# Performance work log

Hardware: AMD Instinct MI355X
Metric: run time of the kernel (lower is better)

## Reference

```python
import jax, jax.numpy as jnp
import numpy as np

N_NODES = 50000
N_EDGES = 650000
NEG_SLOPE = 0.2


def gat_conv(x, src, dst, W, a_src, a_dst, bias, concat):
    """PyG-style GATConv (eval mode, self-loops already included in src/dst).
    x: [N, F_in], W: [F_in, H*C], a_src/a_dst: [H, C], bias: [H*C] or [C]."""
    N = x.shape[0]
    H, C = a_src.shape
    h = (x @ W).reshape(N, H, C)                      # [N, H, C]
    al_src = (h * a_src).sum(-1)                      # [N, H]
    al_dst = (h * a_dst).sum(-1)                      # [N, H]
    logits = jax.nn.leaky_relu(al_src[src] + al_dst[dst], NEG_SLOPE)  # [E, H]
    # segment softmax over destination neighborhoods
    m = jax.ops.segment_max(logits, dst, num_segments=N)
    m = jnp.where(jnp.isfinite(m), m, 0.0)
    e = jnp.exp(logits - m[dst])
    s = jax.ops.segment_sum(e, dst, num_segments=N)
    alpha = e / (s[dst] + 1e-16)                      # [E, H]
    msg = alpha[:, :, None] * h[src]                  # [E, H, C]
    out = jax.ops.segment_sum(msg, dst, num_segments=N)  # [N, H, C]
    out = out.reshape(N, H * C) if concat else out.mean(axis=1)
    return out + bias


def setup_inputs() -> dict:
    key = jax.random.key(0)
    ks = jax.random.split(key, 16)
    IN, HID, H, OUT = 128, 64, 4, 1
    x = jax.random.normal(ks[0], (N_NODES, IN), dtype=jnp.float32)
    edge_index = jax.random.randint(ks[1], (2, N_EDGES), 0, N_NODES, dtype=jnp.int64)
    s = 0.1
    params = {
        'W1': jax.random.normal(ks[2], (IN, H * HID), dtype=jnp.float32) * s,
        'a_src1': jax.random.normal(ks[3], (H, HID), dtype=jnp.float32) * s,
        'a_dst1': jax.random.normal(ks[4], (H, HID), dtype=jnp.float32) * s,
        'b1': jnp.zeros((H * HID,), dtype=jnp.float32),
        'W2': jax.random.normal(ks[5], (H * HID, H * HID), dtype=jnp.float32) * s,
        'a_src2': jax.random.normal(ks[6], (H, HID), dtype=jnp.float32) * s,
        'a_dst2': jax.random.normal(ks[7], (H, HID), dtype=jnp.float32) * s,
        'b2': jnp.zeros((H * HID,), dtype=jnp.float32),
        'W3': jax.random.normal(ks[8], (H * HID, OUT), dtype=jnp.float32) * s,
        'a_src3': jax.random.normal(ks[9], (1, OUT), dtype=jnp.float32) * s,
        'a_dst3': jax.random.normal(ks[10], (1, OUT), dtype=jnp.float32) * s,
        'b3': jnp.zeros((OUT,), dtype=jnp.float32),
    }
    return {'x': x, 'edge_index': edge_index, **params}


def reference(x, edge_index, W1, a_src1, a_dst1, b1, W2, a_src2, a_dst2, b2, W3, a_src3, a_dst3, b3):
    N = x.shape[0]
    loops = jnp.arange(N, dtype=edge_index.dtype)
    src = jnp.concatenate([edge_index[0], loops])
    dst = jnp.concatenate([edge_index[1], loops])
    h = gat_conv(x, src, dst, W1, a_src1, a_dst1, b1, concat=True)
    h = jax.nn.elu(h)  # dropout: identity in eval mode
    h = gat_conv(h, src, dst, W2, a_src2, a_dst2, b2, concat=True)
    h = jax.nn.elu(h)
    out = gat_conv(h, src, dst, W3, a_src3, a_dst3, b3, concat=False)
    return out
```

## Files before the change

### kernel.cpp

```cpp
#include <hip/hip_runtime.h>
#include <math.h>

#define NN 50000
#define NE 650000
#define NET 700000
#define FD 256
#define NEG 0.2f
#define NB 49

static __device__ __forceinline__ float lrelu(float v){ return v > 0.f ? v : NEG*v; }

static __device__ __forceinline__ unsigned short f2bf(float f){
  union { float f; unsigned u; } v; v.f = f;
  unsigned r = v.u + 0x7fff + ((v.u >> 16) & 1);
  return (unsigned short)(r >> 16);
}
static __device__ __forceinline__ float bf2f(unsigned short h){
  union { unsigned u; float f; } v; v.u = ((unsigned)h) << 16;
  return v.f;
}
static __device__ __forceinline__ float bflo(unsigned u){ return __uint_as_float(u << 16); }
static __device__ __forceinline__ float bfhi(unsigned u){ return __uint_as_float(u & 0xffff0000u); }

static __device__ __forceinline__ void gload_lds16(const unsigned short* g, unsigned short* l){
  __builtin_amdgcn_global_load_lds(
      (const __attribute__((address_space(1))) unsigned int*)(g),
      (__attribute__((address_space(3))) unsigned int*)(l), 16, 0, 0);
}

typedef __attribute__((ext_vector_type(8))) short short8_t;
typedef __attribute__((ext_vector_type(4))) float f32x4;

#define NX (NN*128)
#define CAST_ELEMS (NX + 128*256 + 256*256)
#define CAST_BLOCKS ((CAST_ELEMS/4 + 255)/256)
#define CNT_BLOCKS ((NET + 255)/256)
__global__ void init_fused(const float* __restrict__ x, const float* __restrict__ W1,
                           const float* __restrict__ W2,
                           unsigned short* __restrict__ xh, unsigned short* __restrict__ xl,
                           unsigned short* __restrict__ bt1h, unsigned short* __restrict__ bt1l,
                           unsigned short* __restrict__ bt2h, unsigned short* __restrict__ bt2l,
                           const int* __restrict__ ei, int* __restrict__ deg){
  int b = blockIdx.x;
  if (b >= CAST_BLOCKS){
    int e = (b - CAST_BLOCKS)*256 + threadIdx.x;
    if (e < NET){
      int d = (e < NE) ? ei[NE + e] : (e - NE);
      atomicAdd(&deg[d], 1);
    }
    return;
  }
  int i = (b*256 + threadIdx.x)*4;
  if (i < NX){
    float4 f = *(const float4*)(x + i);
    ushort4 h, l;
    h.x = f2bf(f.x); l.x = f2bf(f.x - bf2f(h.x));
    h.y = f2bf(f.y); l.y = f2bf(f.y - bf2f(h.y));
    h.z = f2bf(f.z); l.z = f2bf(f.z - bf2f(h.z));
    h.w = f2bf(f.w); l.w = f2bf(f.w - bf2f(h.w));
    *(ushort4*)(xh + i) = h;
    *(ushort4*)(xl + i) = l;
    return;
  }
  int e, K;
  const float* B;
  unsigned short *bh, *bl;
  if (i < NX + 128*256){ e = i - NX; K = 128; B = W1; bh = bt1h; bl = bt1l; }
  else if (i < CAST_ELEMS){ e = i - NX - 128*256; K = 256; B = W2; bh = bt2h; bl = bt2l; }
  else return;
  int k = e >> 8, n = e & 255;
  float4 f = *(const float4*)(B + e);
  #pragma unroll
  for (int j=0;j<4;j++){
    float fv = (j==0)?f.x:(j==1)?f.y:(j==2)?f.z:f.w;
    unsigned short h = f2bf(fv);
    bh[(n+j)*K + k] = h;
    bl[(n+j)*K + k] = f2bf(fv - bf2f(h));
  }
}

__global__ void scan_block(const int* __restrict__ deg, int* __restrict__ excl, int* __restrict__ bsums){
  __shared__ int sh[256];
  int t = threadIdx.x;
  int i0 = blockIdx.x*1024 + t*4;
  int v0 = (i0+0 < NN) ? deg[i0+0] : 0;
  int v1 = (i0+1 < NN) ? deg[i0+1] : 0;
  int v2 = (i0+2 < NN) ? deg[i0+2] : 0;
  int v3 = (i0+3 < NN) ? deg[i0+3] : 0;
  int tot = v0+v1+v2+v3;
  sh[t] = tot;
  __syncthreads();
  for (int off=1; off<256; off<<=1){
    int x = (t>=off) ? sh[t-off] : 0;
    __syncthreads();
    sh[t] += x;
    __syncthreads();
  }
  int base = sh[t] - tot;
  if (i0+0 < NN) excl[i0+0] = base;
  if (i0+1 < NN) excl[i0+1] = base + v0;
  if (i0+2 < NN) excl[i0+2] = base + v0+v1;
  if (i0+3 < NN) excl[i0+3] = base + v0+v1+v2;
  if (t == 255) bsums[blockIdx.x] = sh[255];
}

__global__ void scan_add(int* __restrict__ indptr, const int* __restrict__ bsums, int* __restrict__ cursor){
  __shared__ int boff[64];
  if (threadIdx.x < 64){
    int lane = threadIdx.x;
    int v = (lane < NB) ? bsums[lane] : 0;
    int orig = v;
    for (int off=1; off<64; off<<=1){
      int u = __shfl_up(v, off);
      if (lane >= off) v += u;
    }
    boff[lane] = v - orig;
  }
  __syncthreads();
  int i = blockIdx.x*blockDim.x + threadIdx.x;
  if (i < NN){
    int v = indptr[i] + boff[i>>10];
    indptr[i] = v;
    cursor[i] = v;
  }
  if (i == 0) indptr[NN] = NET;
}

__global__ void scatter_csr(const int* __restrict__ ei, int* __restrict__ cursor, int* __restrict__ csr){
  int e = blockIdx.x*blockDim.x + threadIdx.x;
  if (e >= NET) return;
  int s, d;
  if (e < NE){ s = ei[e]; d = ei[NE+e]; } else { s = e-NE; d = e-NE; }
  int pos = atomicAdd(&cursor[d], 1);
  csr[pos] = s;
}

template<int K>
__global__ __launch_bounds__(256, 3) void gemm_mfma(const unsigned short* __restrict__ Ahg,
                                                    const unsigned short* __restrict__ Alg,
                                                    const unsigned short* __restrict__ Bth,
                                                    const unsigned short* __restrict__ Btl,
                                                    unsigned short* __restrict__ Cb,
                                                    const float* __restrict__ a_src,
                                                    const float* __restrict__ a_dst,
                                                    float* __restrict__ al,
                                                    int M){
  constexpr int ITERS = K/32;
  __shared__ unsigned short Ah[128*32], Al[128*32], Bh[128*32], Bl[128*32];
  int t = threadIdx.x;
  int wave = t >> 6, lane = t & 63;
  int wm = wave >> 1, wn = wave & 1;
  int quad = lane >> 4, l16 = lane & 15;
  int bm0 = blockIdx.y*128, bn0 = blockIdx.x*128;

  const unsigned short* gsrc = (wave==0)?Ahg:(wave==1)?Alg:(wave==2)?Bth:Btl;
  unsigned short* lbuf       = (wave==0)?Ah :(wave==1)?Al :(wave==2)?Bh :Bl;
  int sbase = (wave < 2) ? bm0 : bn0;
  int srow = lane >> 2;
  int skg  = (lane & 3) * 8;

  const unsigned short* gp[8];
  #pragma unroll
  for (int i=0;i<8;i++){
    int r = sbase + i*16 + srow;
    if (wave < 2) r = min(r, M-1);
    gp[i] = gsrc + (size_t)r*K + skg;
  }

  f32x4 acc[4][4];
  #pragma unroll
  for (int i=0;i<4;i++)
    #pragma unroll
    for (int j=0;j<4;j++) acc[i][j] = (f32x4){0.f,0.f,0.f,0.f};

  #pragma unroll
  for (int i=0;i<8;i++) gload_lds16(gp[i], lbuf + i*512);

  #pragma unroll
  for (int it=0; it<ITERS; ++it){
    __syncthreads();

    short8_t afh[4], afl[4], bfh[4], bfl[4];
    #pragma unroll
    for (int mt=0; mt<4; ++mt){
      int row = wm*64 + mt*16 + l16;
      afh[mt] = *(short8_t*)&Ah[row*32 + quad*8];
      afl[mt] = *(short8_t*)&Al[row*32 + quad*8];
    }
    #pragma unroll
    for (int nt=0; nt<4; ++nt){
      int col = wn*64 + nt*16 + l16;
      bfh[nt] = *(short8_t*)&Bh[col*32 + quad*8];
      bfl[nt] = *(short8_t*)&Bl[col*32 + quad*8];
    }
    __syncthreads();

    if (it+1 < ITERS){
      int k0 = (it+1)*32;
      #pragma unroll
      for (int i=0;i<8;i++) gload_lds16(gp[i] + k0, lbuf + i*512);
    }

    #pragma unroll
    for (int mt=0; mt<4; ++mt)
      #pragma unroll
      for (int nt=0; nt<4; ++nt){
        acc[mt][nt] = __builtin_amdgcn_mfma_f32_16x16x32_bf16(afh[mt], bfh[nt], acc[mt][nt], 0,0,0);
        acc[mt][nt] = __builtin_amdgcn_mfma_f32_16x16x32_bf16(afh[mt], bfl[nt], acc[mt][nt], 0,0,0);
        acc[mt][nt] = __builtin_amdgcn_mfma_f32_16x16x32_bf16(afl[mt], bfh[nt], acc[mt][nt], 0,0,0);
      }
  }

  int head_w = (bn0 >> 6) + wn;
  float cs[4], cd[4];
  #pragma unroll
  for (int nt=0; nt<4; ++nt){
    cs[nt] = a_src[head_w*64 + nt*16 + l16];
    cd[nt] = a_dst[head_w*64 + nt*16 + l16];
  }
  {
    float* fsc = (float*)lbuf;
    int grow = bm0 + wm*64 + lane;
    #pragma unroll
    for (int pass=0; pass<2; ++pass){
      #pragma unroll
      for (int mt=0; mt<4; ++mt)
        #pragma unroll
        for (int r=0; r<4; ++r){
          float p = 0.f;
          #pragma unroll
          for (int nt=0; nt<4; ++nt)
            p += acc[mt][nt][r] * (pass ? cd[nt] : cs[nt]);
          fsc[(mt*16 + quad*4 + r)*17 + l16] = p;
        }
      float s = 0.f;
      #pragma unroll
      for (int j=0; j<16; ++j) s += fsc[lane*17 + j];
      if (grow < M) al[grow*8 + pass*4 + head_w] = s;
    }
  }

  unsigned short* tile = lbuf;
  #pragma unroll
  for (int mt=0; mt<4; ++mt)
    #pragma unroll
    for (int r=0; r<4; ++r){
      int rl = mt*16 + quad*4 + r;
      #pragma unroll
      for (int nt=0; nt<4; ++nt)
        tile[rl*64 + nt*16 + l16] = f2bf(acc[mt][nt][r]);
    }
  int orow = lane >> 3, ocol = (lane & 7) * 8;
  #pragma unroll
  for (int it=0; it<8; ++it){
    int rl = it*8 + orow;
    int row = bm0 + wm*64 + rl;
    if (row < M){
      uint4 v = *(uint4*)&tile[rl*64 + ocol];
      *(uint4*)(Cb + (size_t)row*FD + bn0 + wn*64 + ocol) = v;
    }
  }
}

template<bool FUSE_W3>
__global__ __launch_bounds__(256) void gat_agg(const unsigned short* __restrict__ hb,
                                               const float* __restrict__ al,
                                               const int* __restrict__ indptr, const int* __restrict__ csr,
                                               const float* __restrict__ bias,
                                               unsigned short* __restrict__ outh,
                                               unsigned short* __restrict__ outl,
                                               const float* __restrict__ W3,
                                               float* __restrict__ h3){
  __shared__ float ebuf[8][128];
  __shared__ int   sbuf[8][32];
  int wave = threadIdx.x >> 6, lane = threadIdx.x & 63;
  int half = lane >> 5, l32 = lane & 31;
  int slot = wave*2 + half;
  int n = blockIdx.x*8 + slot;
  if (n >= NN) return;
  int head8 = l32 >> 3;
  int2 ip = *(const int2*)(indptr + n);
  int base = ip.x, deg = ip.y - ip.x;
  float4 ald = *(const float4*)(al + n*8 + 4);
  float* eb = &ebuf[slot][0];
  int*   sb = &sbuf[slot][0];
  const char* hp = (const char*)hb + l32*16;

  float acc[8] = {0.f,0.f,0.f,0.f,0.f,0.f,0.f,0.f};
  float4 esum = make_float4(0.f,0.f,0.f,0.f);

  for (int j0 = 0; j0 < deg; j0 += 32){
    int j = j0 + l32;
    float4 e4 = make_float4(0.f,0.f,0.f,0.f);
    int sj = 0;
    if (j < deg){
      sj = csr[base + j];
      float4 als = *(const float4*)(al + sj*8);
      e4.x = __expf(lrelu(als.x + ald.x));
      e4.y = __expf(lrelu(als.y + ald.y));
      e4.z = __expf(lrelu(als.z + ald.z));
      e4.w = __expf(lrelu(als.w + ald.w));
      esum.x += e4.x; esum.y += e4.y; esum.z += e4.z; esum.w += e4.w;
    }
    *(float4*)&eb[l32*4] = e4;
    sb[l32] = sj << 9;
    int cnt  = min(32, deg - j0);
    int cpad = (cnt + 7) & ~7;
    for (int tt = 0; tt < cpad; tt += 8){
      uint4 r[8];
      float v[8];
      #pragma unroll
      for (int q=0; q<8; ++q){
        int o = sb[tt+q];
        v[q] = eb[(tt+q)*4 + head8];
        r[q] = *(const uint4*)(hp + o);
      }
      #pragma unroll
      for (int q=0; q<8; ++q){
        acc[0]+=v[q]*bflo(r[q].x); acc[1]+=v[q]*bfhi(r[q].x);
        acc[2]+=v[q]*bflo(r[q].y); acc[3]+=v[q]*bfhi(r[q].y);
        acc[4]+=v[q]*bflo(r[q].z); acc[5]+=v[q]*bfhi(r[q].z);
        acc[6]+=v[q]*bflo(r[q].w); acc[7]+=v[q]*bfhi(r[q].w);
      }
    }
  }

  for (int off=16; off; off>>=1){
    esum.x += __shfl_xor(esum.x, off);
    esum.y += __shfl_xor(esum.y, off);
    esum.z += __shfl_xor(esum.z, off);
    esum.w += __shfl_xor(esum.w, off);
  }
  float sH = (head8==0)?esum.x:(head8==1)?esum.y:(head8==2)?esum.z:esum.w;
  float inv = 1.f/(sH + 1e-16f);
  int ch0 = l32*8;
  float4 b0 = *(const float4*)(bias + ch0);
  float4 b1 = *(const float4*)(bias + ch0 + 4);
  float o[8];
  o[0]=acc[0]*inv+b0.x; o[1]=acc[1]*inv+b0.y; o[2]=acc[2]*inv+b0.z; o[3]=acc[3]*inv+b0.w;
  o[4]=acc[4]*inv+b1.x; o[5]=acc[5]*inv+b1.y; o[6]=acc[6]*inv+b1.z; o[7]=acc[7]*inv+b1.w;
  #pragma unroll
  for (int i=0;i<8;i++) o[i] = o[i] > 0.f ? o[i] : expm1f(o[i]);

  if (FUSE_W3){
    float4 w0 = *(const float4*)(W3 + ch0);
    float4 w1 = *(const float4*)(W3 + ch0 + 4);
    float p = o[0]*w0.x + o[1]*w0.y + o[2]*w0.z + o[3]*w0.w
            + o[4]*w1.x + o[5]*w1.y + o[6]*w1.z + o[7]*w1.w;
    #pragma unroll
    for (int off=16; off; off>>=1) p += __shfl_xor(p, off);
    if (l32 == 0) h3[n] = p;
  } else {
    unsigned hi[4], lo[4];
    #pragma unroll
    for (int i=0;i<4;i++){
      unsigned short h0 = f2bf(o[2*i]),   h1 = f2bf(o[2*i+1]);
      unsigned short g0 = f2bf(o[2*i]   - bf2f(h0));
      unsigned short g1 = f2bf(o[2*i+1] - bf2f(h1));
      hi[i] = (unsigned)h0 | ((unsigned)h1 << 16);
      lo[i] = (unsigned)g0 | ((unsigned)g1 << 16);
    }
    *(uint4*)(outh + (size_t)n*FD + ch0) = make_uint4(hi[0],hi[1],hi[2],hi[3]);
    *(uint4*)(outl + (size_t)n*FD + ch0) = make_uint4(lo[0],lo[1],lo[2],lo[3]);
  }
}

__global__ __launch_bounds__(256) void gat_agg3(const float* __restrict__ h3, const int* __restrict__ indptr,
                                                const int* __restrict__ csr, const float* __restrict__ asrc,
                                                const float* __restrict__ adst, const float* __restrict__ b3,
                                                float* __restrict__ out){
  int tid = blockIdx.x*blockDim.x + threadIdx.x;
  int n = tid >> 2, sub = tid & 3;
  if (n >= NN) return;
  float as = asrc[0], ad = adst[0];
  float hd = h3[n]*ad;
  int2 ip = *(const int2*)(indptr + n);
  float s = 0.f, w = 0.f;
  for (int e = ip.x + sub; e < ip.y; e += 4){
    float hv = h3[csr[e]];
    float ee = __expf(lrelu(as*hv + hd));
    s += ee; w += ee*hv;
  }
  s += __shfl_xor(s, 1); w += __shfl_xor(w, 1);
  s += __shfl_xor(s, 2); w += __shfl_xor(w, 2);
  if (sub == 0) out[n] = w/(s + 1e-16f) + b3[0];
}

extern "C" void kernel_launch(void* const* d_in, const int* in_sizes, int n_in,
                              void* d_out, int out_size, void* d_ws, size_t ws_size,
                              hipStream_t stream){
  const float* x   = (const float*)d_in[0];
  const int*   ei  = (const int*)d_in[1];
  const float* W1  = (const float*)d_in[2];
  const float* as1 = (const float*)d_in[3];
  const float* ad1 = (const float*)d_in[4];
  const float* b1  = (const float*)d_in[5];
  const float* W2  = (const float*)d_in[6];
  const float* as2 = (const float*)d_in[7];
  const float* ad2 = (const float*)d_in[8];
  const float* b2  = (const float*)d_in[9];
  const float* W3  = (const float*)d_in[10];
  const float* as3 = (const float*)d_in[11];
  const float* ad3 = (const float*)d_in[12];
  const float* b3  = (const float*)d_in[13];
  float* outp = (float*)d_out;

  char* w = (char*)d_ws;
  size_t off = 0;
  auto alloc = [&](size_t bytes)->void*{
    void* p = w + off; off += (bytes + 255) & ~(size_t)255; return p;
  };
  unsigned short* hb  = (unsigned short*)alloc((size_t)NN*FD*2);
  unsigned short* oh  = (unsigned short*)alloc((size_t)NN*FD*2);
  unsigned short* ol  = (unsigned short*)alloc((size_t)NN*FD*2);
  unsigned short* xh  = (unsigned short*)alloc((size_t)NN*128*2);
  unsigned short* xl  = (unsigned short*)alloc((size_t)NN*128*2);
  float* al    = (float*)alloc((size_t)NN*8*4);
  int*   indptr= (int*)alloc((size_t)(NN+1)*4);
  int*   cursor= (int*)alloc((size_t)NN*4);
  int*   csr   = (int*)alloc((size_t)NET*4);
  int*   bsums = (int*)alloc(64*4);
  float* h3    = (float*)alloc((size_t)NN*4);
  unsigned short* bt1h = (unsigned short*)alloc((size_t)256*128*2);
  unsigned short* bt1l = (unsigned short*)alloc((size_t)256*128*2);
  unsigned short* bt2h = (unsigned short*)alloc((size_t)256*256*2);
  unsigned short* bt2l = (unsigned short*)alloc((size_t)256*256*2);

  hipMemsetAsync(cursor, 0, (size_t)NN*4, stream);
  init_fused<<<CAST_BLOCKS + CNT_BLOCKS, 256, 0, stream>>>(x, W1, W2, xh, xl,
                                                           bt1h, bt1l, bt2h, bt2l,
                                                           ei, cursor);
  scan_block<<<NB, 256, 0, stream>>>(cursor, indptr, bsums);
  scan_add<<<(NN+255)/256, 256, 0, stream>>>(indptr, bsums, cursor);
  scatter_csr<<<(NET+255)/256, 256, 0, stream>>>(ei, cursor, csr);

  dim3 gemm_grid(FD/128, (NN+127)/128);
  int agg_blocks = (NN+7)/8;

  gemm_mfma<128><<<gemm_grid, 256, 0, stream>>>(xh, xl, bt1h, bt1l, hb, as1, ad1, al, NN);
  gat_agg<false><<<agg_blocks, 256, 0, stream>>>(hb, al, indptr, csr, b1, oh, ol, nullptr, nullptr);
  gemm_mfma<256><<<gemm_grid, 256, 0, stream>>>(oh, ol, bt2h, bt2l, hb, as2, ad2, al, NN);
  gat_agg<true><<<agg_blocks, 256, 0, stream>>>(hb, al, indptr, csr, b2, nullptr, nullptr, W3, h3);
  gat_agg3<<<(NN*4+255)/256, 256, 0, stream>>>(h3, indptr, csr, as3, ad3, b3, outp);
}
```

Measured before the change: 343.9 us.

## Split GAT aggregation into edge-alpha pass and panel-partitioned feature gather

The GEMM now writes its bf16 output in eight 32-column panels (panel-major) instead of row-major. A new edge_alpha kernel computes the per-edge exp logits and per-node softmax sums once and stores them. A gather kernel then handles one panel per block with 16 edges in flight per wave, and layer 2 accumulates its W3 projection into h3 with atomics. The aim is a smaller per-panel working set that fits in cache and more gather parallelism. The cost is an extra kernel, the ea buffer written and read back, CSR indices reread eight times, and an extra memset.

```diff
diff --git a/kernel.cpp b/kernel.cpp
--- a/kernel.cpp
+++ b/kernel.cpp
@@ -251,117 +251,151 @@
         tile[rl*64 + nt*16 + l16] = f2bf(acc[mt][nt][r]);
     }
   int orow = lane >> 3, ocol = (lane & 7) * 8;
+  int col0 = bn0 + wn*64 + ocol;
+  int pp = col0 >> 5;
+  unsigned short* pbase = Cb + (size_t)pp*(NN*32) + (col0 & 31);
   #pragma unroll
   for (int it=0; it<8; ++it){
     int rl = it*8 + orow;
     int row = bm0 + wm*64 + rl;
     if (row < M){
       uint4 v = *(uint4*)&tile[rl*64 + ocol];
-      *(uint4*)(Cb + (size_t)row*FD + bn0 + wn*64 + ocol) = v;
-    }
-  }
-}
-
-template<bool FUSE_W3>
-__global__ __launch_bounds__(256) void gat_agg(const unsigned short* __restrict__ hb,
-                                               const float* __restrict__ al,
-                                               const int* __restrict__ indptr, const int* __restrict__ csr,
-                                               const float* __restrict__ bias,
-                                               unsigned short* __restrict__ outh,
-                                               unsigned short* __restrict__ outl,
-                                               const float* __restrict__ W3,
-                                               float* __restrict__ h3){
-  __shared__ float ebuf[8][128];
-  __shared__ int   sbuf[8][32];
+      *(uint4*)(pbase + (size_t)row*32) = v;
+    }
+  }
+}
+
+__global__ __launch_bounds__(256) void edge_alpha(const float* __restrict__ al,
+                                                  const int* __restrict__ indptr,
+                                                  const int* __restrict__ csr,
+                                                  float* __restrict__ ea,
+                                                  float* __restrict__ esum){
   int wave = threadIdx.x >> 6, lane = threadIdx.x & 63;
-  int half = lane >> 5, l32 = lane & 31;
-  int slot = wave*2 + half;
-  int n = blockIdx.x*8 + slot;
+  int n = blockIdx.x*4 + wave;
   if (n >= NN) return;
-  int head8 = l32 >> 3;
   int2 ip = *(const int2*)(indptr + n);
   int base = ip.x, deg = ip.y - ip.x;
   float4 ald = *(const float4*)(al + n*8 + 4);
-  float* eb = &ebuf[slot][0];
-  int*   sb = &sbuf[slot][0];
-  const char* hp = (const char*)hb + l32*16;
-
-  float acc[8] = {0.f,0.f,0.f,0.f,0.f,0.f,0.f,0.f};
-  float4 esum = make_float4(0.f,0.f,0.f,0.f);
-
-  for (int j0 = 0; j0 < deg; j0 += 32){
-    int j = j0 + l32;
-    float4 e4 = make_float4(0.f,0.f,0.f,0.f);
-    int sj = 0;
+  float4 es = make_float4(0.f,0.f,0.f,0.f);
+  for (int j0 = 0; j0 < deg; j0 += 64){
+    int j = j0 + lane;
     if (j < deg){
-      sj = csr[base + j];
+      int sj = csr[base + j];
       float4 als = *(const float4*)(al + sj*8);
+      float4 e4;
       e4.x = __expf(lrelu(als.x + ald.x));
       e4.y = __expf(lrelu(als.y + ald.y));
       e4.z = __expf(lrelu(als.z + ald.z));
       e4.w = __expf(lrelu(als.w + ald.w));
-      esum.x += e4.x; esum.y += e4.y; esum.z += e4.z; esum.w += e4.w;
-    }
-    *(float4*)&eb[l32*4] = e4;
-    sb[l32] = sj << 9;
-    int cnt  = min(32, deg - j0);
-    int cpad = (cnt + 7) & ~7;
-    for (int tt = 0; tt < cpad; tt += 8){
-      uint4 r[8];
-      float v[8];
-      #pragma unroll
-      for (int q=0; q<8; ++q){
-        int o = sb[tt+q];
-        v[q] = eb[(tt+q)*4 + head8];
-        r[q] = *(const uint4*)(hp + o);
+      ea[0*NET + base + j] = e4.x;
+      ea[1*NET + base + j] = e4.y;
+      ea[2*NET + base + j] = e4.z;
+      ea[3*NET + base + j] = e4.w;
+      es.x += e4.x; es.y += e4.y; es.z += e4.z; es.w += e4.w;
+    }
+  }
+  for (int off=32; off; off>>=1){
+    es.x += __shfl_xor(es.x, off);
+    es.y += __shfl_xor(es.y, off);
+    es.z += __shfl_xor(es.z, off);
+    es.w += __shfl_xor(es.w, off);
+  }
+  if (lane == 0) *(float4*)(esum + n*4) = es;
+}
+
+template<bool FUSE_W3>
+__global__ __launch_bounds__(256) void gat_gather(const unsigned short* __restrict__ hb,
+                                                  const float* __restrict__ ea,
+                                                  const float* __restrict__ esum,
+                                                  const int* __restrict__ indptr,
+                                                  const int* __restrict__ csr,
+                                                  const float* __restrict__ bias,
+                                                  unsigned short* __restrict__ outh,
+                                                  unsigned short* __restrict__ outl,
+                                                  const float* __restrict__ W3,
+                                                  float* __restrict__ h3){
+  __shared__ float ebuf[4][64];
+  __shared__ int   sbuf[4][64];
+  int wave = threadIdx.x >> 6, lane = threadIdx.x & 63;
+  int p = blockIdx.x & 7;
+  int n = (blockIdx.x >> 3)*4 + wave;
+  if (n >= NN) return;
+  int hp = p >> 1;
+  int q = lane >> 2, r16 = (lane & 3)*16;
+  int2 ip = *(const int2*)(indptr + n);
+  int base = ip.x, deg = ip.y - ip.x;
+  float inv = 1.f/(esum[n*4 + hp] + 1e-16f);
+  const char* pb = (const char*)(hb + (size_t)p*(NN*32)) + r16;
+  const float* eap = ea + (size_t)hp*NET;
+  float* eb = &ebuf[wave][0];
+  int*   sb = &sbuf[wave][0];
+
+  float acc[8] = {0.f,0.f,0.f,0.f,0.f,0.f,0.f,0.f};
+
+  for (int j0 = 0; j0 < deg; j0 += 64){
+    int j = j0 + lane;
+    float a = 0.f; int sj = 0;
+    if (j < deg){ sj = csr[base + j]; a = eap[base + j]; }
+    eb[lane] = a;
+    sb[lane] = sj << 6;
+    int cnt = min(64, deg - j0);
+    int nst = (cnt + 15) >> 4;
+    uint4 u[4]; float av[4];
+    #pragma unroll
+    for (int s=0; s<4; ++s){
+      if (s < nst){
+        int e = s*16 + q;
+        av[s] = eb[e];
+        u[s] = *(const uint4*)(pb + sb[e]);
+      } else { av[s] = 0.f; u[s] = make_uint4(0,0,0,0); }
+    }
+    #pragma unroll
+    for (int s=0; s<4; ++s){
+      acc[0]+=av[s]*bflo(u[s].x); acc[1]+=av[s]*bfhi(u[s].x);
+      acc[2]+=av[s]*bflo(u[s].y); acc[3]+=av[s]*bfhi(u[s].y);
+      acc[4]+=av[s]*bflo(u[s].z); acc[5]+=av[s]*bfhi(u[s].z);
+      acc[6]+=av[s]*bflo(u[s].w); acc[7]+=av[s]*bfhi(u[s].w);
+    }
+  }
+
+  #pragma unroll
+  for (int i=0;i<8;i++){
+    acc[i] += __shfl_xor(acc[i], 4);
+    acc[i] += __shfl_xor(acc[i], 8);
+    acc[i] += __shfl_xor(acc[i], 16);
+    acc[i] += __shfl_xor(acc[i], 32);
+  }
+
+  if (lane < 4){
+    int ch0 = p*32 + lane*8;
+    float4 b0 = *(const float4*)(bias + ch0);
+    float4 b1 = *(const float4*)(bias + ch0 + 4);
+    float o[8];
+    o[0]=acc[0]*inv+b0.x; o[1]=acc[1]*inv+b0.y; o[2]=acc[2]*inv+b0.z; o[3]=acc[3]*inv+b0.w;
+    o[4]=acc[4]*inv+b1.x; o[5]=acc[5]*inv+b1.y; o[6]=acc[6]*inv+b1.z; o[7]=acc[7]*inv+b1.w;
+    #pragma unroll
+    for (int i=0;i<8;i++) o[i] = o[i] > 0.f ? o[i] : expm1f(o[i]);
+    if (FUSE_W3){
+      float4 w0 = *(const float4*)(W3 + ch0);
+      float4 w1 = *(const float4*)(W3 + ch0 + 4);
+      float pp = o[0]*w0.x + o[1]*w0.y + o[2]*w0.z + o[3]*w0.w
+               + o[4]*w1.x + o[5]*w1.y + o[6]*w1.z + o[7]*w1.w;
+      pp += __shfl_xor(pp, 1);
+      pp += __shfl_xor(pp, 2);
+      if (lane == 0) atomicAdd(h3 + n, pp);
+    } else {
+      unsigned hi[4], lo[4];
+      #pragma unroll
+      for (int i=0;i<4;i++){
+        unsigned short h0 = f2bf(o[2*i]),   h1 = f2bf(o[2*i+1]);
+        unsigned short g0 = f2bf(o[2*i]   - bf2f(h0));
+        unsigned short g1 = f2bf(o[2*i+1] - bf2f(h1));
+        hi[i] = (unsigned)h0 | ((unsigned)h1 << 16);
+        lo[i] = (unsigned)g0 | ((unsigned)g1 << 16);
       }
-      #pragma unroll
-      for (int q=0; q<8; ++q){
-        acc[0]+=v[q]*bflo(r[q].x); acc[1]+=v[q]*bfhi(r[q].x);
-        acc[2]+=v[q]*bflo(r[q].y); acc[3]+=v[q]*bfhi(r[q].y);
-        acc[4]+=v[q]*bflo(r[q].z); acc[5]+=v[q]*bfhi(r[q].z);
-        acc[6]+=v[q]*bflo(r[q].w); acc[7]+=v[q]*bfhi(r[q].w);
-      }
-    }
-  }
-
-  for (int off=16; off; off>>=1){
-    esum.x += __shfl_xor(esum.x, off);
-    esum.y += __shfl_xor(esum.y, off);
-    esum.z += __shfl_xor(esum.z, off);
-    esum.w += __shfl_xor(esum.w, off);
-  }
-  float sH = (head8==0)?esum.x:(head8==1)?esum.y:(head8==2)?esum.z:esum.w;
-  float inv = 1.f/(sH + 1e-16f);
-  int ch0 = l32*8;
-  float4 b0 = *(const float4*)(bias + ch0);
-  float4 b1 = *(const float4*)(bias + ch0 + 4);
-  float o[8];
-  o[0]=acc[0]*inv+b0.x; o[1]=acc[1]*inv+b0.y; o[2]=acc[2]*inv+b0.z; o[3]=acc[3]*inv+b0.w;
-  o[4]=acc[4]*inv+b1.x; o[5]=acc[5]*inv+b1.y; o[6]=acc[6]*inv+b1.z; o[7]=acc[7]*inv+b1.w;
-  #pragma unroll
-  for (int i=0;i<8;i++) o[i] = o[i] > 0.f ? o[i] : expm1f(o[i]);
-
-  if (FUSE_W3){
-    float4 w0 = *(const float4*)(W3 + ch0);
-    float4 w1 = *(const float4*)(W3 + ch0 + 4);
-    float p = o[0]*w0.x + o[1]*w0.y + o[2]*w0.z + o[3]*w0.w
-            + o[4]*w1.x + o[5]*w1.y + o[6]*w1.z + o[7]*w1.w;
-    #pragma unroll
-    for (int off=16; off; off>>=1) p += __shfl_xor(p, off);
-    if (l32 == 0) h3[n] = p;
-  } else {
-    unsigned hi[4], lo[4];
-    #pragma unroll
-    for (int i=0;i<4;i++){
-      unsigned short h0 = f2bf(o[2*i]),   h1 = f2bf(o[2*i+1]);
-      unsigned short g0 = f2bf(o[2*i]   - bf2f(h0));
-      unsigned short g1 = f2bf(o[2*i+1] - bf2f(h1));
-      hi[i] = (unsigned)h0 | ((unsigned)h1 << 16);
-      lo[i] = (unsigned)g0 | ((unsigned)g1 << 16);
-    }
-    *(uint4*)(outh + (size_t)n*FD + ch0) = make_uint4(hi[0],hi[1],hi[2],hi[3]);
-    *(uint4*)(outl + (size_t)n*FD + ch0) = make_uint4(lo[0],lo[1],lo[2],lo[3]);
+      *(uint4*)(outh + (size_t)n*FD + ch0) = make_uint4(hi[0],hi[1],hi[2],hi[3]);
+      *(uint4*)(outl + (size_t)n*FD + ch0) = make_uint4(lo[0],lo[1],lo[2],lo[3]);
+    }
   }
 }
 
@@ -416,6 +450,8 @@
   unsigned short* xh  = (unsigned short*)alloc((size_t)NN*128*2);
   unsigned short* xl  = (unsigned short*)alloc((size_t)NN*128*2);
   float* al    = (float*)alloc((size_t)NN*8*4);
+  float* ea    = (float*)alloc((size_t)4*NET*4);
+  float* esum  = (float*)alloc((size_t)NN*4*4);
   int*   indptr= (int*)alloc((size_t)(NN+1)*4);
   int*   cursor= (int*)alloc((size_t)NN*4);
   int*   csr   = (int*)alloc((size_t)NET*4);
@@ -427,6 +463,7 @@
   unsigned short* bt2l = (unsigned short*)alloc((size_t)256*256*2);
 
   hipMemsetAsync(cursor, 0, (size_t)NN*4, stream);
+  hipMemsetAsync(h3, 0, (size_t)NN*4, stream);
   init_fused<<<CAST_BLOCKS + CNT_BLOCKS, 256, 0, stream>>>(x, W1, W2, xh, xl,
                                                            bt1h, bt1l, bt2h, bt2l,
                                                            ei, cursor);
@@ -435,11 +472,14 @@
   scatter_csr<<<(NET+255)/256, 256, 0, stream>>>(ei, cursor, csr);
 
   dim3 gemm_grid(FD/128, (NN+127)/128);
-  int agg_blocks = (NN+7)/8;
+  int na_blocks = (NN+3)/4;
+  int gather_blocks = na_blocks*8;
 
   gemm_mfma<128><<<gemm_grid, 256, 0, stream>>>(xh, xl, bt1h, bt1l, hb, as1, ad1, al, NN);
-  gat_agg<false><<<agg_blocks, 256, 0, stream>>>(hb, al, indptr, csr, b1, oh, ol, nullptr, nullptr);
+  edge_alpha<<<na_blocks, 256, 0, stream>>>(al, indptr, csr, ea, esum);
+  gat_gather<false><<<gather_blocks, 256, 0, stream>>>(hb, ea, esum, indptr, csr, b1, oh, ol, nullptr, nullptr);
   gemm_mfma<256><<<gemm_grid, 256, 0, stream>>>(oh, ol, bt2h, bt2l, hb, as2, ad2, al, NN);
-  gat_agg<true><<<agg_blocks, 256, 0, stream>>>(hb, al, indptr, csr, b2, nullptr, nullptr, W3, h3);
+  edge_alpha<<<na_blocks, 256, 0, stream>>>(al, indptr, csr, ea, esum);
+  gat_gather<true><<<gather_blocks, 256, 0, stream>>>(hb, ea, esum, indptr, csr, b2, nullptr, nullptr, W3, h3);
   gat_agg3<<<(NN*4+255)/256, 256, 0, stream>>>(h3, indptr, csr, as3, ad3, b3, outp);
 }
```

After: 671.3 us. 1.95x slower.
